# Optimization experiments

Measured on AMD Instinct MI355X. Metric: run time of the kernel, lower is better.

The kernel has to match this reference:

```python
import jax, jax.numpy as jnp
import numpy as np

EPS = 1e-6
BASE_LR = 0.01
MAX_GRAD_NORM = 1.0
CHUNK = 32


def _rms(x, w):
    return x * jax.lax.rsqrt(jnp.mean(x * x, axis=-1, keepdims=True) + EPS) * w


def _mem_fwd(p, x):
    # Memory MLP: linear -> silu -> linear -> RMSNorm -> residual. x: [D]
    h = jax.nn.silu(p['W1'] @ x)
    o = p['W2'] @ h
    return x + _rms(o, p['ln'])


def _loss(p, k, v, w):
    pred = _mem_fwd(p, k)
    return jnp.mean((v - pred) ** 2 * w)


def _binop(a, b):
    # Mamba-like: (a_j*a_i, kv_j + a_j*kv_i)  == torch.addcmul(kv_j, a_j, kv_i)
    (ai, ki), (aj, kj) = a, b
    return (aj * ai, kj + aj * ki)


def _scan_update(past_s, past_m, g, eta, alpha):
    # past_s/past_m: [B,*shape]; g: [B,C,*shape]; eta/alpha: [B,C]
    ext = (1,) * (g.ndim - 2)
    eta_b = eta.reshape(eta.shape + ext)
    alpha_b = alpha.reshape(alpha.shape + ext)
    ones = jnp.ones_like(eta_b[:, :1])
    a = jnp.concatenate([ones, eta_b], axis=1)
    kv = jnp.concatenate([past_s[:, None], -g], axis=1)
    _, s = jax.lax.associative_scan(_binop, (a, kv), axis=1)  # S_t = eta_t*S_{t-1} - g_t
    beta = jnp.concatenate([ones, 1.0 - alpha_b], axis=1)
    mem = jnp.concatenate([past_m[:, None], s[:, 1:]], axis=1)
    _, m = jax.lax.associative_scan(_binop, (beta, mem), axis=1)  # M_t = beta_t*M_{t-1} + S_t
    return s[:, -1], m[:, -1]


def _forward(x, wq, wk, wv, q_norm_w, k_norm_w, alpha_w, theta_w, eta_w, mem_w1, mem_w2, mem_ln):
    B, S, D = x.shape
    NC = S // CHUNK
    params = {'W1': jnp.broadcast_to(mem_w1, (B,) + mem_w1.shape),
              'W2': jnp.broadcast_to(mem_w2, (B,) + mem_w2.shape),
              'ln': jnp.broadcast_to(mem_ln, (B,) + mem_ln.shape)}
    surpr = jax.tree.map(jnp.zeros_like, params)
    xc_all = x.reshape(B, NC, CHUNK, D).transpose(1, 0, 2, 3)  # [NC,B,C,D]
    # per-sample, per-token grad of the TTT loss w.r.t. memory params
    grad_fn = jax.vmap(jax.vmap(jax.grad(_loss), in_axes=(None, 0, 0, 0)),
                       in_axes=(0, 0, 0, 0))

    def step(carry, xc):
        params, surpr = carry
        k = _rms(jax.nn.silu(xc @ wk.T), k_norm_w)      # [B,C,D]
        v = jax.nn.silu(xc @ wv.T)                       # [B,C,D]
        theta = BASE_LR * jax.nn.sigmoid(xc @ theta_w.T)  # [B,C,1] adaptive lr as loss weight
        alpha = jax.nn.sigmoid(xc @ alpha_w.T)[..., 0]     # [B,C] forget gate
        eta = jax.nn.sigmoid(xc @ eta_w.T)[..., 0]         # [B,C] momentum decay
        g = grad_fn(params, k, v, theta)                  # leaves [B,C,*shape]
        # global grad-norm clip per (b, t)
        sq = sum(jnp.sum(gi * gi, axis=tuple(range(2, gi.ndim)))
                 for gi in jax.tree.leaves(g))
        coef = jnp.minimum(MAX_GRAD_NORM / (jnp.sqrt(sq) + 1e-6), 1.0)
        g = jax.tree.map(lambda gi: gi * coef.reshape(coef.shape + (1,) * (gi.ndim - 2)), g)
        new_s, new_p = {}, {}
        for n in params:
            s_n, m_n = _scan_update(surpr[n], params[n], g[n], eta, alpha)
            new_s[n], new_p[n] = s_n, m_n
        return (new_p, new_s), None

    (params, surpr), _ = jax.lax.scan(step, (params, surpr), xc_all)
    # retrieve from the final memory weights
    q = _rms(jax.nn.silu(x @ wq.T), q_norm_w)
    h = jax.nn.silu(jnp.einsum('bsd,bid->bsi', q, params['W1']))
    o = jnp.einsum('bsi,bdi->bsd', h, params['W2'])
    out = q + _rms(o, params['ln'][:, None, :])
    return out


def setup_inputs() -> dict:
    key = jax.random.key(0)
    ks = jax.random.split(key, 12)
    B, S, D, I = 4, 512, 512, 1024

    def xavier(k, shape):
        fan = shape[-1] + shape[-2] if len(shape) > 1 else 2 * shape[-1]
        return jax.random.uniform(k, shape, jnp.float32, -1.0, 1.0) * jnp.sqrt(6.0 / fan)

    return {
        'x': jax.random.normal(ks[0], (B, S, D), jnp.float32),
        'wq': xavier(ks[1], (D, D)),
        'wk': xavier(ks[2], (D, D)),
        'wv': xavier(ks[3], (D, D)),
        'q_norm_w': jnp.ones((D,), jnp.float32),
        'k_norm_w': jnp.ones((D,), jnp.float32),
        'alpha_w': xavier(ks[4], (1, D)),
        'theta_w': xavier(ks[5], (1, D)),
        'eta_w': xavier(ks[6], (1, D)),
        'mem_w1': xavier(ks[7], (I, D)),
        'mem_w2': xavier(ks[8], (D, I)),
        'mem_ln': jnp.ones((D,), jnp.float32),
    }


def reference(x, wq, wk, wv, q_norm_w, k_norm_w, alpha_w, theta_w, eta_w, mem_w1, mem_w2, mem_ln):
    return _forward(x, wq, wk, wv, q_norm_w, k_norm_w, alpha_w, theta_w, eta_w,
                    mem_w1, mem_w2, mem_ln)
```

## Files before the change

kernel.cpp:

```cpp
#include <hip/hip_runtime.h>
#include <hip/hip_bf16.h>

#define B_ 4
#define S_ 512
#define D_ 512
#define I_ 1024
#define C_ 32
#define NC_ 16

#define KBUF (B_*S_*D_)
#define STSZ (B_*I_*D_)
#define HSZ  (B_*I_*C_)
#define DOSZ (B_*C_*D_)
#define OFF_K    0
#define OFF_V    (OFF_K + KBUF)
#define OFF_Q    (OFF_V + KBUF)
#define OFF_TH   (OFF_Q + KBUF)
#define OFF_AL   (OFF_TH + B_*S_)
#define OFF_ET   (OFF_AL + B_*S_)
#define OFF_KN2  (OFF_ET + B_*S_)
#define OFF_SLN  (OFF_KN2 + B_*S_)
#define OFF_MLN  (OFF_SLN + B_*D_)
#define OFF_H2   (OFF_MLN + B_*D_)
#define OFF_Z1   (OFF_H2 + 2*HSZ)
#define OFF_DHP  (OFF_Z1 + HSZ)
#define OFF_DO   (OFF_DHP + HSZ)
#define OFF_DLN  (OFF_DO + DOSZ)
#define OFF_OB   (OFF_DLN + DOSZ)
#define OFF_SLAB (OFF_OB + DOSZ)
#define SLABSTR  256
#define OFF_TICK (OFF_SLAB + NC_*B_*SLABSTR)
#define OFF_FLAG (OFF_TICK + 64)
#define OFF_ORET (OFF_FLAG + 16)
#define OFF_BST  (OFF_ORET + KBUF)
#define OFF_KBFf (OFF_BST + 2*STSZ)
#define OFF_KBTf (OFF_KBFf + KBUF/2)
#define OFF_HIT  (OFF_KBTf + KBUF/2)
#define OFF_HTI  (OFF_HIT + HSZ)
#define OFF_DOB  (OFF_HTI + HSZ)
#define OFF_DOT  (OFF_DOB + DOSZ/2)

typedef __attribute__((ext_vector_type(8))) short s8v;
typedef __attribute__((ext_vector_type(4))) float f4v;

__device__ __forceinline__ float bf2f(__hip_bfloat16 v){ return __bfloat162float(v); }
__device__ __forceinline__ float bfu2f(unsigned short u){ return __uint_as_float(((unsigned)u)<<16); }
__device__ __forceinline__ unsigned short f2bfu(float f){
  unsigned x = __float_as_uint(f);
  return (unsigned short)((x + 0x7FFFu + ((x>>16)&1u)) >> 16);
}
__device__ __forceinline__ float4 u42f4(ushort4 u){
  float4 r; r.x=bfu2f(u.x); r.y=bfu2f(u.y); r.z=bfu2f(u.z); r.w=bfu2f(u.w); return r;
}
__device__ __forceinline__ ushort4 f42u4(float4 v){
  ushort4 r; r.x=f2bfu(v.x); r.y=f2bfu(v.y); r.z=f2bfu(v.z); r.w=f2bfu(v.w); return r;
}
__device__ __forceinline__ float ldin(const void* p, size_t i, int f){
  return f ? ((const float*)p)[i] : bf2f(((const __hip_bfloat16*)p)[i]);
}
__device__ __forceinline__ float4 ld4g(const void* p, size_t i, int f){
  if(f) return ((const float4*)p)[i>>2];
  return u42f4(((const ushort4*)p)[i>>2]);
}
__device__ __forceinline__ void unp8(uint4 u, float* f){
  f[0]=bfu2f((unsigned short)(u.x&0xffffu)); f[1]=bfu2f((unsigned short)(u.x>>16));
  f[2]=bfu2f((unsigned short)(u.y&0xffffu)); f[3]=bfu2f((unsigned short)(u.y>>16));
  f[4]=bfu2f((unsigned short)(u.z&0xffffu)); f[5]=bfu2f((unsigned short)(u.z>>16));
  f[6]=bfu2f((unsigned short)(u.w&0xffffu)); f[7]=bfu2f((unsigned short)(u.w>>16));
}
__device__ __forceinline__ uint4 pck8(const float* f){
  uint4 u;
  u.x = (unsigned)f2bfu(f[0]) | ((unsigned)f2bfu(f[1])<<16);
  u.y = (unsigned)f2bfu(f[2]) | ((unsigned)f2bfu(f[3])<<16);
  u.z = (unsigned)f2bfu(f[4]) | ((unsigned)f2bfu(f[5])<<16);
  u.w = (unsigned)f2bfu(f[6]) | ((unsigned)f2bfu(f[7])<<16);
  return u;
}

__device__ __forceinline__ float blockReduceSum(float v, float* sm){
  #pragma unroll
  for(int o=32;o>0;o>>=1) v += __shfl_down(v,o,64);
  int wid = threadIdx.x>>6, lane = threadIdx.x&63;
  __syncthreads();
  if(lane==0) sm[wid]=v;
  __syncthreads();
  return sm[0]+sm[1]+sm[2]+sm[3];
}

__global__ void d0_detect(const void* __restrict__ x, float* __restrict__ ws){
  __shared__ int cnt;
  if(threadIdx.x==0) cnt=0;
  __syncthreads();
  unsigned w = ((const unsigned*)x)[(size_t)threadIdx.x*931 + 17];
  int e = (w>>7)&0xFF;
  if(e>=110 && e<=140) atomicAdd(&cnt,1);
  __syncthreads();
  if(threadIdx.x==0) ((int*)(ws+OFF_FLAG))[0] = (cnt<32) ? 1 : 0;
}

__global__ void p0_init(float* __restrict__ ws, const void* __restrict__ w1,
                        const void* __restrict__ w2, const void* __restrict__ ln){
  int f = ((const int*)(ws+OFF_FLAG))[0];
  unsigned short* bst = (unsigned short*)(ws + OFF_BST);
  size_t id = (size_t)blockIdx.x*blockDim.x + threadIdx.x;
  size_t stride = (size_t)gridDim.x*blockDim.x;
  ushort4 z4 = {0,0,0,0};
  for(size_t t4=id; t4<(size_t)(STSZ/4); t4+=stride){
    size_t e4 = t4 % (size_t)(I_*D_/4);
    *(ushort4*)(bst + (size_t)STSZ + t4*4)   = f42u4(ld4g(w1, e4*4, f));
    *(ushort4*)(bst + (size_t)3*STSZ + t4*4) = f42u4(ld4g(w2, e4*4, f));
    *(ushort4*)(bst + t4*4) = z4;
    *(ushort4*)(bst + (size_t)2*STSZ + t4*4) = z4;
  }
  for(size_t t=id; t<(size_t)(B_*D_); t+=stride){
    ws[OFF_MLN+t] = ldin(ln,t % D_,f);
    ws[OFF_SLN+t] = 0.f;
  }
  for(size_t t=id; t<(size_t)(NC_*B_*SLABSTR); t+=stride) ws[OFF_SLAB+t]=0.f;
  int* tick = (int*)(ws + OFF_TICK);
  for(size_t t=id; t<64; t+=stride) tick[t]=0;
}

__global__ void __launch_bounds__(256) cvt_in(const void* __restrict__ x,
                    const void* __restrict__ wk, const void* __restrict__ wv,
                    const void* __restrict__ wq, float* __restrict__ ws){
  int f = ((const int*)(ws+OFF_FLAG))[0];
  unsigned short* xbf = (unsigned short*)(ws + OFF_ORET);
  unsigned short* wbf = (unsigned short*)(ws + OFF_KBFf);
  size_t id = (size_t)blockIdx.x*blockDim.x + threadIdx.x;
  size_t stride = (size_t)gridDim.x*blockDim.x;
  for(size_t t4=id; t4<(size_t)(KBUF/4); t4+=stride)
    *(ushort4*)(xbf + t4*4) = f42u4(ld4g(x, t4*4, f));
  for(size_t t4=id; t4<(size_t)(3*D_*D_/4); t4+=stride){
    int pid = (int)(t4 / (D_*D_/4));
    size_t e4 = t4 % (size_t)(D_*D_/4);
    const void* W = (pid==0)?wk:((pid==1)?wv:wq);
    *(ushort4*)(wbf + t4*4) = f42u4(ld4g(W, e4*4, f));
  }
}

__global__ void __launch_bounds__(256) p1a(float* __restrict__ ws){
  const unsigned short* xbf = (const unsigned short*)(ws + OFF_ORET);
  const unsigned short* wbf = (const unsigned short*)(ws + OFF_KBFf);
  int pid = blockIdx.z;
  float* outp = ws + ((pid==0)?OFF_K:((pid==1)?OFF_V:OFF_Q));
  const unsigned short* W = wbf + (size_t)pid*D_*D_;
  int r0 = blockIdx.x*64, j0 = blockIdx.y*64;
  int w = threadIdx.x>>6, lane = threadIdx.x&63;
  int col = lane&15, lg = lane>>4;
  f4v acc[4] = {{0,0,0,0},{0,0,0,0},{0,0,0,0},{0,0,0,0}};
  for(int k0=0;k0<512;k0+=32){
    s8v bB = __builtin_bit_cast(s8v, *(const uint4*)(W + (size_t)(j0 + w*16 + col)*512 + k0 + lg*8));
    #pragma unroll
    for(int rg=0;rg<4;rg++){
      s8v aA = __builtin_bit_cast(s8v, *(const uint4*)(xbf + (size_t)(r0 + rg*16 + col)*512 + k0 + lg*8));
      acc[rg] = __builtin_amdgcn_mfma_f32_16x16x32_bf16(aA, bB, acc[rg], 0,0,0);
    }
  }
  #pragma unroll
  for(int rg=0;rg<4;rg++)
    #pragma unroll
    for(int j=0;j<4;j++){
      float z = acc[rg][j];
      outp[(size_t)(r0 + rg*16 + lg*4 + j)*512 + j0 + w*16 + col] = z/(1.f+expf(-z));
    }
}

__global__ void __launch_bounds__(256) p1b(const void* __restrict__ x,
                    const void* __restrict__ kn,
                    const void* __restrict__ qn,
                    const void* __restrict__ aw,
                    const void* __restrict__ tw,
                    const void* __restrict__ ew,
                    float* __restrict__ ws){
  int f = ((const int*)(ws+OFF_FLAG))[0];
  int tok = blockIdx.x; int tid = threadIdx.x;
  __shared__ float sm[8];
  float* krow = ws + OFF_K + (size_t)tok*512;
  float* qrow = ws + OFF_Q + (size_t)tok*512;
  float a = krow[tid], b = krow[tid+256];
  float ss = blockReduceSum(a*a+b*b, sm);
  float n = rsqrtf(ss*(1.f/512.f) + 1e-6f);
  float k1v = a*n*ldin(kn,tid,f);
  float k2v = b*n*ldin(kn,tid+256,f);
  krow[tid]=k1v; krow[tid+256]=k2v;
  float kn2 = blockReduceSum(k1v*k1v+k2v*k2v, sm);
  if(tid==0) ws[OFF_KN2+tok]=kn2;
  a = qrow[tid]; b = qrow[tid+256];
  ss = blockReduceSum(a*a+b*b, sm);
  n = rsqrtf(ss*(1.f/512.f)+1e-6f);
  qrow[tid]=a*n*ldin(qn,tid,f);
  qrow[tid+256]=b*n*ldin(qn,tid+256,f);
  float x1=ldin(x,(size_t)tok*512+tid,f), x2=ldin(x,(size_t)tok*512+tid+256,f);
  float td = blockReduceSum(x1*ldin(tw,tid,f) + x2*ldin(tw,tid+256,f), sm);
  float ad = blockReduceSum(x1*ldin(aw,tid,f) + x2*ldin(aw,tid+256,f), sm);
  float ed = blockReduceSum(x1*ldin(ew,tid,f) + x2*ldin(ew,tid+256,f), sm);
  if(tid==0){
    ws[OFF_TH+tok] = 0.01f/(1.f+expf(-td));
    ws[OFF_AL+tok] = 1.f/(1.f+expf(-ad));
    ws[OFF_ET+tok] = 1.f/(1.f+expf(-ed));
  }
}

__global__ void __launch_bounds__(256) tr_k(float* __restrict__ ws){
  unsigned short* kbf = (unsigned short*)(ws + OFF_KBFf);
  unsigned short* kbt = (unsigned short*)(ws + OFF_KBTf);
  int b = blockIdx.z, st = blockIdx.y, dt = blockIdx.x;
  int s0 = st*64, d0 = dt*64;
  __shared__ unsigned short t[64][72];
  int tid = threadIdx.x;
  #pragma unroll
  for(int q=0;q<4;q++){
    int idx = tid + q*256; int r = idx>>4, cq = idx&15;
    float4 v = *(const float4*)(ws + OFF_K + ((size_t)(b*512 + s0 + r))*512 + d0 + cq*4);
    ushort4 u; u.x=f2bfu(v.x); u.y=f2bfu(v.y); u.z=f2bfu(v.z); u.w=f2bfu(v.w);
    *(ushort4*)&t[r][cq*4] = u;
    *(ushort4*)(kbf + ((size_t)(b*512 + s0 + r))*512 + d0 + cq*4) = u;
  }
  __syncthreads();
  #pragma unroll
  for(int q=0;q<4;q++){
    int idx = tid + q*256; int d = idx>>4, sq = idx&15;
    ushort4 u; u.x=t[sq*4+0][d]; u.y=t[sq*4+1][d]; u.z=t[sq*4+2][d]; u.w=t[sq*4+3][d];
    *(ushort4*)(kbt + ((size_t)(b*512 + d0 + d))*512 + s0 + sq*4) = u;
  }
}

__global__ void __launch_bounds__(256) k1_w1(float* __restrict__ ws, int c){
  unsigned short* bsw1 = (unsigned short*)(ws + OFF_BST);
  unsigned short* bmw1 = bsw1 + STSZ;
  const unsigned short* kbf = (const unsigned short*)(ws + OFF_KBFf);
  const unsigned short* kbt = (const unsigned short*)(ws + OFF_KBTf);
  int b = blockIdx.y, bx = blockIdx.x, tid = threadIdx.x;
  __shared__ float sE[32], sC[32], scal[3];
  if(c>0){
    const float* slab = ws + OFF_SLAB + ((long)(c-1)*B_ + b)*SLABSTR;
    if(tid<32){ sE[tid]=slab[128+tid]; sC[tid]=slab[160+tid]; }
    if(tid>=32 && tid<35) scal[tid-32]=slab[192+(tid-32)];
  }
  __syncthreads();
  float PE = c>0? scal[0]:1.f, PB = c>0? scal[1]:1.f, Q = c>0? scal[2]:0.f;
  if(bx==64){
    if(c>0){
      for(int d=tid; d<512; d+=256){
        float gE=0,gC=0;
        for(int u=0;u<32;u++){
          float dl = ws[OFF_DLN + ((size_t)(b*32+u))*512 + d];
          gE += sE[u]*dl; gC += sC[u]*dl;
        }
        size_t ix = OFF_SLN + (size_t)b*512 + d;
        float sv=ws[ix], mv=ws[ix + (OFF_MLN-OFF_SLN)];
        ws[ix] = PE*sv - gE;
        ws[ix + (OFF_MLN-OFF_SLN)] = PB*mv + Q*sv - gC;
      }
    }
    return;
  }
  __shared__ __align__(16) float gbf[4][2][16][36];
  __shared__ __align__(16) unsigned short ztile[4][16][40];
  __shared__ __align__(16) float zred[4][16][32];
  __shared__ float hredL[32];
  int w = tid>>6, lane = tid&63;
  int i0 = bx*16;
  int col = lane&15, lg = lane>>4;
  int rr = lane>>2, c0 = (lane&3)*8;
  s8v aE = {}, aC = {};
  if(c>0){
    const float* dp = ws + OFF_DHP + ((size_t)(b*I_ + i0 + col))*32 + lg*8;
    float4 dv0 = *(const float4*)dp;
    float4 dv1 = *(const float4*)(dp+4);
    float dv[8] = {dv0.x,dv0.y,dv0.z,dv0.w,dv1.x,dv1.y,dv1.z,dv1.w};
    #pragma unroll
    for(int j=0;j<8;j++){
      aE[j] = (short)f2bfu(sE[lg*8+j]*dv[j]);
      aC[j] = (short)f2bfu(sC[lg*8+j]*dv[j]);
    }
  }
  f4v zacc0 = {0.f,0.f,0.f,0.f}, zacc1 = {0.f,0.f,0.f,0.f};
  const int d0w = w*128;
  const size_t srowbase = ((size_t)(b*I_ + i0))*512;
  const size_t kprow = (size_t)(c-1)*32;
  for(int sl=0; sl<4; sl++){
    int dbase = d0w + sl*32;
    size_t gaddr = srowbase + (size_t)rr*512 + dbase + c0;
    if(c>0){
      #pragma unroll
      for(int t2=0;t2<2;t2++){
        int dt = dbase + t2*16;
        const unsigned short* kp = kbt + ((size_t)(b*512 + dt + col))*512 + kprow + lg*8;
        s8v kB = __builtin_bit_cast(s8v, *(const uint4*)kp);
        f4v zero4 = {0.f,0.f,0.f,0.f};
        f4v gE4 = __builtin_amdgcn_mfma_f32_16x16x32_bf16(aE, kB, zero4, 0,0,0);
        f4v gC4 = __builtin_amdgcn_mfma_f32_16x16x32_bf16(aC, kB, zero4, 0,0,0);
        #pragma unroll
        for(int j=0;j<4;j++){
          gbf[w][0][lg*4+j][t2*16+col] = gE4[j];
          gbf[w][1][lg*4+j][t2*16+col] = gC4[j];
        }
      }
      uint4 su = *(uint4*)(bsw1 + gaddr);
      uint4 mu = *(uint4*)(bmw1 + gaddr);
      float s8[8], m8[8];
      unp8(su, s8); unp8(mu, m8);
      float ns[8], nmv[8];
      #pragma unroll
      for(int j=0;j<8;j++){
        float ge = gbf[w][0][rr][c0+j];
        float gc = gbf[w][1][rr][c0+j];
        ns[j]  = PE*s8[j] - ge;
        nmv[j] = PB*m8[j] + Q*s8[j] - gc;
      }
      *(uint4*)(bsw1 + gaddr) = pck8(ns);
      uint4 nmu = pck8(nmv);
      *(uint4*)(bmw1 + gaddr) = nmu;
      *(uint4*)&ztile[w][rr][c0] = nmu;
    } else {
      uint4 mu = *(uint4*)(bmw1 + gaddr);
      *(uint4*)&ztile[w][rr][c0] = mu;
    }
    if(c<16){
      s8v mA = __builtin_bit_cast(s8v, *(const uint4*)&ztile[w][col][lg*8]);
      const unsigned short* kc0 = kbf + ((size_t)(b*512 + c*32 + col))*512 + dbase + lg*8;
      s8v kB0 = __builtin_bit_cast(s8v, *(const uint4*)kc0);
      s8v kB1 = __builtin_bit_cast(s8v, *(const uint4*)(kc0 + (size_t)16*512));
      zacc0 = __builtin_amdgcn_mfma_f32_16x16x32_bf16(mA, kB0, zacc0, 0,0,0);
      zacc1 = __builtin_amdgcn_mfma_f32_16x16x32_bf16(mA, kB1, zacc1, 0,0,0);
    }
  }
  if(c<16){
    #pragma unroll
    for(int j=0;j<4;j++){
      zred[w][lg*4+j][col]    = zacc0[j];
      zred[w][lg*4+j][16+col] = zacc1[j];
    }
    if(tid<32) hredL[tid]=0.f;
    __syncthreads();
    unsigned short* hit = (unsigned short*)(ws + OFF_HIT) + (size_t)(c&1)*HSZ;
    unsigned short* hti = (unsigned short*)(ws + OFF_HTI) + (size_t)(c&1)*HSZ;
    #pragma unroll
    for(int e=0;e<2;e++){
      int idx = tid*2+e; int row = idx>>5, t = idx&31;
      float z = zred[0][row][t]+zred[1][row][t]+zred[2][row][t]+zred[3][row][t];
      size_t zb = ((size_t)(b*I_ + i0 + row))*32 + t;
      ws[OFF_Z1+zb] = z;
      float h = z/(1.f+expf(-z));
      unsigned short hb = f2bfu(h);
      hit[zb] = hb;
      hti[((size_t)(b*C_+t))*I_ + i0 + row] = hb;
      atomicAdd(&hredL[t], h*h);
    }
    __syncthreads();
    if(tid<32) atomicAdd(ws + OFF_SLAB + ((size_t)c*B_ + b)*SLABSTR + tid, hredL[tid]);
  }
}

__global__ void __launch_bounds__(256) k2_w2(float* __restrict__ ws, int c){
  unsigned short* bsw2 = (unsigned short*)(ws + OFF_BST) + (size_t)2*STSZ;
  unsigned short* bmw2 = bsw2 + STSZ;
  const unsigned short* hitp = (const unsigned short*)(ws + OFF_HIT) + (size_t)((c-1)&1)*HSZ;
  const unsigned short* htic = (const unsigned short*)(ws + OFF_HTI) + (size_t)(c&1)*HSZ;
  const unsigned short* dotb = (const unsigned short*)(ws + OFF_DOT);
  int b = blockIdx.y, bx = blockIdx.x, tid = threadIdx.x;
  int d0 = bx*16;
  __shared__ float sE[32], sC[32], scal[3];
  __shared__ __align__(16) float gbf[4][2][16][36];
  __shared__ __align__(16) unsigned short ztile[4][16][40];
  __shared__ __align__(16) float ored[4][16][32];
  if(c>0){
    const float* slab = ws + OFF_SLAB + ((long)(c-1)*B_+b)*SLABSTR;
    if(tid<32){ sE[tid]=slab[128+tid]; sC[tid]=slab[160+tid]; }
    if(tid>=32&&tid<35) scal[tid-32]=slab[192+tid-32];
  }
  __syncthreads();
  float PE = c>0?scal[0]:1.f, PB=c>0?scal[1]:1.f, Q=c>0?scal[2]:0.f;
  int w = tid>>6, lane = tid&63;
  int col = lane&15, lg = lane>>4;
  int rr = lane>>2, c0 = (lane&3)*8;
  s8v aE = {}, aC = {};
  if(c>0){
    const unsigned short* dp = dotb + ((size_t)(b*D_ + d0 + col))*32 + lg*8;
    float dv[8]; unp8(*(const uint4*)dp, dv);
    #pragma unroll
    for(int j=0;j<8;j++){
      aE[j] = (short)f2bfu(sE[lg*8+j]*dv[j]);
      aC[j] = (short)f2bfu(sC[lg*8+j]*dv[j]);
    }
  }
  f4v oacc0 = {0.f,0.f,0.f,0.f}, oacc1 = {0.f,0.f,0.f,0.f};
  const size_t srowbase = ((size_t)(b*D_ + d0))*1024;
  size_t ga0 = srowbase + (size_t)rr*1024 + w*256 + c0;
  uint4 su={0,0,0,0}, mu, svn=su, mvn;
  if(c>0) su = *(uint4*)(bsw2 + ga0);
  mu = *(uint4*)(bmw2 + ga0);
  for(int sl=0; sl<8; sl++){
    int ibase = w*256 + sl*32;
    size_t gaddr = srowbase + (size_t)rr*1024 + ibase + c0;
    if(sl<7){
      if(c>0) svn = *(uint4*)(bsw2 + gaddr + 32);
      mvn = *(uint4*)(bmw2 + gaddr + 32);
    }
    if(c>0){
      #pragma unroll
      for(int t2=0;t2<2;t2++){
        const unsigned short* hp = hitp + ((size_t)(b*I_ + ibase + t2*16 + col))*32 + lg*8;
        s8v hB = __builtin_bit_cast(s8v, *(const uint4*)hp);
        f4v zero4 = {0.f,0.f,0.f,0.f};
        f4v gE4 = __builtin_amdgcn_mfma_f32_16x16x32_bf16(aE, hB, zero4, 0,0,0);
        f4v gC4 = __builtin_amdgcn_mfma_f32_16x16x32_bf16(aC, hB, zero4, 0,0,0);
        #pragma unroll
        for(int j=0;j<4;j++){
          gbf[w][0][lg*4+j][t2*16+col] = gE4[j];
          gbf[w][1][lg*4+j][t2*16+col] = gC4[j];
        }
      }
      float s8[8], m8[8];
      unp8(su, s8); unp8(mu, m8);
      float ns[8], nmv[8];
      #pragma unroll
      for(int j=0;j<8;j++){
        ns[j]  = PE*s8[j] - gbf[w][0][rr][c0+j];
        nmv[j] = PB*m8[j] + Q*s8[j] - gbf[w][1][rr][c0+j];
      }
      *(uint4*)(bsw2 + gaddr) = pck8(ns);
      uint4 nmu = pck8(nmv);
      *(uint4*)(bmw2 + gaddr) = nmu;
      *(uint4*)&ztile[w][rr][c0] = nmu;
    } else {
      *(uint4*)&ztile[w][rr][c0] = mu;
    }
    if(c<16){
      s8v mA = __builtin_bit_cast(s8v, *(const uint4*)&ztile[w][col][lg*8]);
      const unsigned short* hb = htic + ((size_t)(b*C_+col))*I_ + ibase + lg*8;
      s8v hB0 = __builtin_bit_cast(s8v, *(const uint4*)hb);
      s8v hB1 = __builtin_bit_cast(s8v, *(const uint4*)(hb + (size_t)16*I_));
      oacc0 = __builtin_amdgcn_mfma_f32_16x16x32_bf16(mA, hB0, oacc0, 0,0,0);
      oacc1 = __builtin_amdgcn_mfma_f32_16x16x32_bf16(mA, hB1, oacc1, 0,0,0);
    }
    su = svn; mu = mvn;
  }
  if(c<16){
    #pragma unroll
    for(int j=0;j<4;j++){
      ored[w][lg*4+j][col]    = oacc0[j];
      ored[w][lg*4+j][16+col] = oacc1[j];
    }
    __syncthreads();
    #pragma unroll
    for(int e=0;e<2;e++){
      int idx = tid*2+e; int row = idx>>5, t = idx&31;
      float o = ored[0][row][t]+ored[1][row][t]+ored[2][row][t]+ored[3][row][t];
      ws[OFF_OB + ((size_t)(b*C_+t))*512 + d0 + row] = o;
    }
  }
}

__global__ void __launch_bounds__(256) k3_rms(float* __restrict__ ws, int c){
  int t = blockIdx.x, b = blockIdx.y, tid=threadIdx.x;
  __shared__ float sm[8];
  int tok = b*S_ + c*32 + t;
  const float* orow = ws + OFF_OB + ((size_t)(b*32+t))*512;
  const float* krow = ws + OFF_K + (size_t)tok*512;
  const float* vrow = ws + OFF_V + (size_t)tok*512;
  const float* lrow = ws + OFF_MLN + (size_t)b*512;
  float th = ws[OFF_TH + tok];
  float o1=orow[tid], o2=orow[tid+256];
  float mu = blockReduceSum(o1*o1+o2*o2, sm)*(1.f/512.f);
  float n = rsqrtf(mu + 1e-6f);
  float l1=lrow[tid], l2=lrow[tid+256];
  float k1=krow[tid], k2=krow[tid+256];
  float v1=vrow[tid], v2=vrow[tid+256];
  float c2 = 2.f*th*(1.f/512.f);
  float u1 = c2*(k1 + o1*n*l1 - v1);
  float u2 = c2*(k2 + o2*n*l2 - v2);
  float s1 = blockReduceSum(u1*l1*o1 + u2*l2*o2, sm);
  float dln1 = u1*o1*n, dln2v = u2*o2*n;
  float f = n*n*n*s1*(1.f/512.f);
  float do1 = n*l1*u1 - f*o1;
  float do2 = n*l2*u2 - f*o2;
  float don2 = blockReduceSum(do1*do1+do2*do2, sm);
  float dl2s = blockReduceSum(dln1*dln1+dln2v*dln2v, sm);
  float* dorow = ws + OFF_DO + ((size_t)(b*32+t))*512;
  float* dlrow = ws + OFF_DLN + ((size_t)(b*32+t))*512;
  dorow[tid]=do1; dorow[tid+256]=do2;
  dlrow[tid]=dln1; dlrow[tid+256]=dln2v;
  unsigned short* dob = (unsigned short*)(ws + OFF_DOB);
  unsigned short* dotb = (unsigned short*)(ws + OFF_DOT);
  dob[((size_t)(b*C_+t))*512 + tid]       = f2bfu(do1);
  dob[((size_t)(b*C_+t))*512 + tid + 256] = f2bfu(do2);
  dotb[((size_t)(b*D_ + tid))*32 + t]       = f2bfu(do1);
  dotb[((size_t)(b*D_ + tid + 256))*32 + t] = f2bfu(do2);
  if(tid==0){
    float* slab = ws + OFF_SLAB + ((size_t)c*B_+b)*SLABSTR;
    slab[64+t]=don2; slab[96+t]=dl2s;
  }
}

__global__ void __launch_bounds__(256) k4_dh(float* __restrict__ ws, int c){
  unsigned short* bmw2 = (unsigned short*)(ws + OFF_BST) + (size_t)3*STSZ;
  const unsigned short* dob = (const unsigned short*)(ws + OFF_DOB);
  int bx = blockIdx.x, b = blockIdx.y, tid = threadIdx.x;
  int i0 = bx*16;
  __shared__ unsigned short m2u[16][520];
  __shared__ __align__(16) float dred[4][16][32];
  __shared__ float red[32], coefl[32], bsufl[32];
  __shared__ int lastf;
  #pragma unroll
  for(int q=0;q<4;q++){
    int idx = tid + q*256; int d = idx>>1, half = idx&1;
    uint4 v = *(const uint4*)(bmw2 + ((size_t)(b*D_+d))*1024 + i0 + half*8);
    unsigned short tmp[8]; *(uint4*)tmp = v;
    #pragma unroll
    for(int jj=0;jj<8;jj++) m2u[half*8+jj][d] = tmp[jj];
  }
  if(tid<32) red[tid]=0.f;
  __syncthreads();
  int w = tid>>6, lane = tid&63;
  int col = lane&15, lg = lane>>4;
  f4v acc0 = {0.f,0.f,0.f,0.f}, acc1 = {0.f,0.f,0.f,0.f};
  #pragma unroll
  for(int ks=0;ks<4;ks++){
    int k0 = w*128 + ks*32;
    s8v mA = __builtin_bit_cast(s8v, *(const uint4*)&m2u[col][k0 + lg*8]);
    const unsigned short* dp = dob + ((size_t)(b*C_+col))*512 + k0 + lg*8;
    s8v dB0 = __builtin_bit_cast(s8v, *(const uint4*)dp);
    s8v dB1 = __builtin_bit_cast(s8v, *(const uint4*)(dp + (size_t)16*512));
    acc0 = __builtin_amdgcn_mfma_f32_16x16x32_bf16(mA, dB0, acc0, 0,0,0);
    acc1 = __builtin_amdgcn_mfma_f32_16x16x32_bf16(mA, dB1, acc1, 0,0,0);
  }
  #pragma unroll
  for(int j=0;j<4;j++){
    dred[w][lg*4+j][col]    = acc0[j];
    dred[w][lg*4+j][16+col] = acc1[j];
  }
  __syncthreads();
  #pragma unroll
  for(int e=0;e<2;e++){
    int idx = tid*2+e; int row = idx>>5, t = idx&31;
    float dh = dred[0][row][t]+dred[1][row][t]+dred[2][row][t]+dred[3][row][t];
    size_t zb = ((size_t)(b*I_ + i0 + row))*32 + t;
    float z = ws[OFF_Z1+zb];
    float s = 1.f/(1.f+expf(-z));
    float dp_ = dh * s*(1.f + z*(1.f-s));
    ws[OFF_DHP+zb] = dp_;
    atomicAdd(&red[t], dp_*dp_);
  }
  __syncthreads();
  float* slab = ws + OFF_SLAB + ((size_t)c*B_+b)*SLABSTR;
  if(tid<32) atomicAdd(&slab[32+tid], red[tid]);
  __threadfence();
  __syncthreads();
  if(tid==0){
    int* tick = (int*)(ws+OFF_TICK);
    lastf = (atomicAdd(&tick[c*B_+b],1) == 63) ? 1 : 0;
  }
  __syncthreads();
  if(!lastf) return;
  if(tid<32){
    float sqd = atomicAdd(&slab[32+tid], 0.f);
    float hn  = atomicAdd(&slab[0+tid], 0.f);
    float don2 = slab[64+tid], dl2 = slab[96+tid];
    float kn2 = ws[OFF_KN2 + b*S_ + c*32 + tid];
    float sq = sqd*kn2 + don2*hn + dl2;
    coefl[tid] = fminf(1.f/(sqrtf(sq)+1e-6f), 1.f);
  }
  __syncthreads();
  if(tid==0){
    const float* eta = ws + OFF_ET + b*S_ + c*32;
    const float* alp = ws + OFF_AL + b*S_ + c*32;
    float Esuf=1.f, Bsuf=1.f, cu=1.f;
    for(int u=31;u>=0;u--){
      if(u<31){
        float e1 = eta[u+1], b1 = 1.f-alp[u+1];
        Esuf *= e1; Bsuf *= b1;
        cu = Bsuf + e1*cu;
      }
      bsufl[u]=Bsuf;
      slab[128+u] = Esuf*coefl[u];
      slab[160+u] = cu*coefl[u];
    }
    float PE = Esuf*eta[0];
    float PB = Bsuf*(1.f-alp[0]);
    float Q=0.f, Epre=1.f;
    for(int t2=0;t2<32;t2++){ Epre *= eta[t2]; Q += bsufl[t2]*Epre; }
    slab[192]=PE; slab[193]=PB; slab[194]=Q;
  }
}

__global__ void __launch_bounds__(256) cvt_q(float* __restrict__ ws){
  unsigned short* qbf = (unsigned short*)(ws + OFF_V);
  size_t id = (size_t)blockIdx.x*blockDim.x + threadIdx.x;
  float4 v = *(const float4*)(ws + OFF_Q + id*4);
  *(ushort4*)(qbf + id*4) = f42u4(v);
}

__global__ void __launch_bounds__(256) r1_gemm(float* __restrict__ ws){
  const unsigned short* qbf = (const unsigned short*)(ws + OFF_V);
  const unsigned short* bmw1 = (const unsigned short*)(ws + OFF_BST) + STSZ;
  unsigned short* hqb = (unsigned short*)(ws + OFF_K);
  int b = blockIdx.z;
  int s0 = blockIdx.x*64, i0 = blockIdx.y*64;
  int w = threadIdx.x>>6, lane = threadIdx.x&63;
  int col = lane&15, lg = lane>>4;
  const unsigned short* qb = qbf + (size_t)b*S_*D_;
  const unsigned short* w1b = bmw1 + (size_t)b*I_*D_;
  f4v acc[4] = {{0,0,0,0},{0,0,0,0},{0,0,0,0},{0,0,0,0}};
  for(int k0=0;k0<512;k0+=32){
    s8v bB = __builtin_bit_cast(s8v, *(const uint4*)(w1b + (size_t)(i0 + w*16 + col)*512 + k0 + lg*8));
    #pragma unroll
    for(int rg=0;rg<4;rg++){
      s8v aA = __builtin_bit_cast(s8v, *(const uint4*)(qb + (size_t)(s0 + rg*16 + col)*512 + k0 + lg*8));
      acc[rg] = __builtin_amdgcn_mfma_f32_16x16x32_bf16(aA, bB, acc[rg], 0,0,0);
    }
  }
  unsigned short* hb = hqb + (size_t)b*S_*I_;
  #pragma unroll
  for(int rg=0;rg<4;rg++)
    #pragma unroll
    for(int j=0;j<4;j++){
      float z = acc[rg][j];
      hb[(size_t)(s0 + rg*16 + lg*4 + j)*1024 + i0 + w*16 + col] = f2bfu(z/(1.f+expf(-z)));
    }
}

__global__ void __launch_bounds__(256) r2_gemm(float* __restrict__ ws){
  const unsigned short* hqb = (const unsigned short*)(ws + OFF_K);
  const unsigned short* bmw2 = (const unsigned short*)(ws + OFF_BST) + (size_t)3*STSZ;
  int b=blockIdx.z;
  int s0=blockIdx.x*64, d0=blockIdx.y*64;
  int w = threadIdx.x>>6, lane = threadIdx.x&63;
  int col = lane&15, lg = lane>>4;
  const unsigned short* hb = hqb + (size_t)b*S_*I_;
  const unsigned short* w2b = bmw2 + (size_t)b*D_*I_;
  f4v acc[4] = {{0,0,0,0},{0,0,0,0},{0,0,0,0},{0,0,0,0}};
  for(int k0=0;k0<1024;k0+=32){
    s8v bB = __builtin_bit_cast(s8v, *(const uint4*)(w2b + (size_t)(d0 + w*16 + col)*1024 + k0 + lg*8));
    #pragma unroll
    for(int rg=0;rg<4;rg++){
      s8v aA = __builtin_bit_cast(s8v, *(const uint4*)(hb + (size_t)(s0 + rg*16 + col)*1024 + k0 + lg*8));
      acc[rg] = __builtin_amdgcn_mfma_f32_16x16x32_bf16(aA, bB, acc[rg], 0,0,0);
    }
  }
  float* od = ws + OFF_ORET + (size_t)b*S_*D_;
  #pragma unroll
  for(int rg=0;rg<4;rg++)
    #pragma unroll
    for(int j=0;j<4;j++)
      od[(size_t)(s0 + rg*16 + lg*4 + j)*512 + d0 + w*16 + col] = acc[rg][j];
}

__global__ void __launch_bounds__(256) r3_out(float* __restrict__ ws, void* __restrict__ out){
  int f = ((const int*)(ws+OFF_FLAG))[0];
  int tok=blockIdx.x, tid=threadIdx.x;
  int b = tok >> 9;
  __shared__ float sm[8];
  const float* orow = ws + OFF_ORET + (size_t)tok*512;
  const float* qrow = ws + OFF_Q + (size_t)tok*512;
  const float* lrow = ws + OFF_MLN + (size_t)b*512;
  float o1=orow[tid], o2=orow[tid+256];
  float mu = blockReduceSum(o1*o1+o2*o2, sm)*(1.f/512.f);
  float n = rsqrtf(mu+1e-6f);
  float r1v = qrow[tid]     + o1*n*lrow[tid];
  float r2v = qrow[tid+256] + o2*n*lrow[tid+256];
  if(f){
    ((float*)out)[(size_t)tok*512+tid]     = r1v;
    ((float*)out)[(size_t)tok*512+tid+256] = r2v;
  } else {
    ((__hip_bfloat16*)out)[(size_t)tok*512+tid]     = __float2bfloat16(r1v);
    ((__hip_bfloat16*)out)[(size_t)tok*512+tid+256] = __float2bfloat16(r2v);
  }
}

extern "C" void kernel_launch(void* const* d_in, const int* in_sizes, int n_in,
                              void* d_out, int out_size, void* d_ws, size_t ws_size,
                              hipStream_t stream) {
  const void* x  = d_in[0];
  const void* wq = d_in[1];
  const void* wk = d_in[2];
  const void* wv = d_in[3];
  const void* qn = d_in[4];
  const void* kn = d_in[5];
  const void* aw = d_in[6];
  const void* tw = d_in[7];
  const void* ew = d_in[8];
  const void* w1 = d_in[9];
  const void* w2 = d_in[10];
  const void* ln = d_in[11];
  float* ws = (float*)d_ws;

  d0_detect<<<1,64,0,stream>>>(x, ws);
  p0_init<<<2048,256,0,stream>>>(ws, w1, w2, ln);
  cvt_in<<<2048,256,0,stream>>>(x, wk, wv, wq, ws);
  p1a<<<dim3(32,8,3),256,0,stream>>>(ws);
  p1b<<<2048,256,0,stream>>>(x, kn, qn, aw, tw, ew, ws);
  tr_k<<<dim3(8,8,4),256,0,stream>>>(ws);
  for(int c=0;c<=16;c++){
    k1_w1<<<dim3(65,4),256,0,stream>>>(ws, c);
    k2_w2<<<dim3(32,4),256,0,stream>>>(ws, c);
    if(c<16){
      k3_rms<<<dim3(32,4),256,0,stream>>>(ws, c);
      k4_dh<<<dim3(64,4),256,0,stream>>>(ws, c);
    }
  }
  cvt_q<<<1024,256,0,stream>>>(ws);
  r1_gemm<<<dim3(8,16,4),256,0,stream>>>(ws);
  r2_gemm<<<dim3(8,8,4),256,0,stream>>>(ws);
  r3_out<<<2048,256,0,stream>>>(ws, d_out);
}
```

Baseline: 1.056 ms.

## Fuse RMS-backward into dh kernel and merge conversion launches

```diff
diff --git a/kernel.cpp b/kernel.cpp
--- a/kernel.cpp
+++ b/kernel.cpp
@@ -30,7 +30,8 @@
 #define OFF_SLAB (OFF_OB + DOSZ)
 #define SLABSTR  256
 #define OFF_TICK (OFF_SLAB + NC_*B_*SLABSTR)
-#define OFF_FLAG (OFF_TICK + 64)
+#define OFF_TK2  (OFF_TICK + 64)
+#define OFF_FLAG (OFF_TK2 + 128)
 #define OFF_ORET (OFF_FLAG + 16)
 #define OFF_BST  (OFF_ORET + KBUF)
 #define OFF_KBFf (OFF_BST + 2*STSZ)
@@ -87,6 +88,12 @@
   return sm[0]+sm[1]+sm[2]+sm[3];
 }
 
+__device__ __forceinline__ float wred(float v){
+  #pragma unroll
+  for(int o=32;o>0;o>>=1) v += __shfl_xor(v,o,64);
+  return v;
+}
+
 __global__ void d0_detect(const void* __restrict__ x, float* __restrict__ ws){
   __shared__ int cnt;
   if(threadIdx.x==0) cnt=0;
@@ -99,7 +106,9 @@
 }
 
 __global__ void p0_init(float* __restrict__ ws, const void* __restrict__ w1,
-                        const void* __restrict__ w2, const void* __restrict__ ln){
+                        const void* __restrict__ w2, const void* __restrict__ ln,
+                        const void* __restrict__ x, const void* __restrict__ wk,
+                        const void* __restrict__ wv, const void* __restrict__ wq){
   int f = ((const int*)(ws+OFF_FLAG))[0];
   unsigned short* bst = (unsigned short*)(ws + OFF_BST);
   size_t id = (size_t)blockIdx.x*blockDim.x + threadIdx.x;
@@ -112,23 +121,8 @@
     *(ushort4*)(bst + t4*4) = z4;
     *(ushort4*)(bst + (size_t)2*STSZ + t4*4) = z4;
   }
-  for(size_t t=id; t<(size_t)(B_*D_); t+=stride){
-    ws[OFF_MLN+t] = ldin(ln,t % D_,f);
-    ws[OFF_SLN+t] = 0.f;
-  }
-  for(size_t t=id; t<(size_t)(NC_*B_*SLABSTR); t+=stride) ws[OFF_SLAB+t]=0.f;
-  int* tick = (int*)(ws + OFF_TICK);
-  for(size_t t=id; t<64; t+=stride) tick[t]=0;
-}
-
-__global__ void __launch_bounds__(256) cvt_in(const void* __restrict__ x,
-                    const void* __restrict__ wk, const void* __restrict__ wv,
-                    const void* __restrict__ wq, float* __restrict__ ws){
-  int f = ((const int*)(ws+OFF_FLAG))[0];
   unsigned short* xbf = (unsigned short*)(ws + OFF_ORET);
   unsigned short* wbf = (unsigned short*)(ws + OFF_KBFf);
-  size_t id = (size_t)blockIdx.x*blockDim.x + threadIdx.x;
-  size_t stride = (size_t)gridDim.x*blockDim.x;
   for(size_t t4=id; t4<(size_t)(KBUF/4); t4+=stride)
     *(ushort4*)(xbf + t4*4) = f42u4(ld4g(x, t4*4, f));
   for(size_t t4=id; t4<(size_t)(3*D_*D_/4); t4+=stride){
@@ -137,6 +131,13 @@
     const void* W = (pid==0)?wk:((pid==1)?wv:wq);
     *(ushort4*)(wbf + t4*4) = f42u4(ld4g(W, e4*4, f));
   }
+  for(size_t t=id; t<(size_t)(B_*D_); t+=stride){
+    ws[OFF_MLN+t] = ldin(ln,t % D_,f);
+    ws[OFF_SLN+t] = 0.f;
+  }
+  for(size_t t=id; t<(size_t)(NC_*B_*SLABSTR); t+=stride) ws[OFF_SLAB+t]=0.f;
+  int* tick = (int*)(ws + OFF_TICK);
+  for(size_t t=id; t<192; t+=stride) tick[t]=0;
 }
 
 __global__ void __launch_bounds__(256) p1a(float* __restrict__ ws){
@@ -189,8 +190,12 @@
   a = qrow[tid]; b = qrow[tid+256];
   ss = blockReduceSum(a*a+b*b, sm);
   n = rsqrtf(ss*(1.f/512.f)+1e-6f);
-  qrow[tid]=a*n*ldin(qn,tid,f);
-  qrow[tid+256]=b*n*ldin(qn,tid+256,f);
+  float q1 = a*n*ldin(qn,tid,f);
+  float q2 = b*n*ldin(qn,tid+256,f);
+  qrow[tid]=q1; qrow[tid+256]=q2;
+  unsigned short* qbf = (unsigned short*)(ws + OFF_ORET + KBUF/2);
+  qbf[(size_t)tok*512+tid]     = f2bfu(q1);
+  qbf[(size_t)tok*512+tid+256] = f2bfu(q2);
   float x1=ldin(x,(size_t)tok*512+tid,f), x2=ldin(x,(size_t)tok*512+tid+256,f);
   float td = blockReduceSum(x1*ldin(tw,tid,f) + x2*ldin(tw,tid+256,f), sm);
   float ad = blockReduceSum(x1*ldin(aw,tid,f) + x2*ldin(aw,tid+256,f), sm);
@@ -454,56 +459,16 @@
   }
 }
 
-__global__ void __launch_bounds__(256) k3_rms(float* __restrict__ ws, int c){
-  int t = blockIdx.x, b = blockIdx.y, tid=threadIdx.x;
-  __shared__ float sm[8];
-  int tok = b*S_ + c*32 + t;
-  const float* orow = ws + OFF_OB + ((size_t)(b*32+t))*512;
-  const float* krow = ws + OFF_K + (size_t)tok*512;
-  const float* vrow = ws + OFF_V + (size_t)tok*512;
-  const float* lrow = ws + OFF_MLN + (size_t)b*512;
-  float th = ws[OFF_TH + tok];
-  float o1=orow[tid], o2=orow[tid+256];
-  float mu = blockReduceSum(o1*o1+o2*o2, sm)*(1.f/512.f);
-  float n = rsqrtf(mu + 1e-6f);
-  float l1=lrow[tid], l2=lrow[tid+256];
-  float k1=krow[tid], k2=krow[tid+256];
-  float v1=vrow[tid], v2=vrow[tid+256];
-  float c2 = 2.f*th*(1.f/512.f);
-  float u1 = c2*(k1 + o1*n*l1 - v1);
-  float u2 = c2*(k2 + o2*n*l2 - v2);
-  float s1 = blockReduceSum(u1*l1*o1 + u2*l2*o2, sm);
-  float dln1 = u1*o1*n, dln2v = u2*o2*n;
-  float f = n*n*n*s1*(1.f/512.f);
-  float do1 = n*l1*u1 - f*o1;
-  float do2 = n*l2*u2 - f*o2;
-  float don2 = blockReduceSum(do1*do1+do2*do2, sm);
-  float dl2s = blockReduceSum(dln1*dln1+dln2v*dln2v, sm);
-  float* dorow = ws + OFF_DO + ((size_t)(b*32+t))*512;
-  float* dlrow = ws + OFF_DLN + ((size_t)(b*32+t))*512;
-  dorow[tid]=do1; dorow[tid+256]=do2;
-  dlrow[tid]=dln1; dlrow[tid+256]=dln2v;
-  unsigned short* dob = (unsigned short*)(ws + OFF_DOB);
-  unsigned short* dotb = (unsigned short*)(ws + OFF_DOT);
-  dob[((size_t)(b*C_+t))*512 + tid]       = f2bfu(do1);
-  dob[((size_t)(b*C_+t))*512 + tid + 256] = f2bfu(do2);
-  dotb[((size_t)(b*D_ + tid))*32 + t]       = f2bfu(do1);
-  dotb[((size_t)(b*D_ + tid + 256))*32 + t] = f2bfu(do2);
-  if(tid==0){
-    float* slab = ws + OFF_SLAB + ((size_t)c*B_+b)*SLABSTR;
-    slab[64+t]=don2; slab[96+t]=dl2s;
-  }
-}
-
-__global__ void __launch_bounds__(256) k4_dh(float* __restrict__ ws, int c){
+__global__ void __launch_bounds__(256) k34(float* __restrict__ ws, int c){
   unsigned short* bmw2 = (unsigned short*)(ws + OFF_BST) + (size_t)3*STSZ;
-  const unsigned short* dob = (const unsigned short*)(ws + OFF_DOB);
   int bx = blockIdx.x, b = blockIdx.y, tid = threadIdx.x;
   int i0 = bx*16;
-  __shared__ unsigned short m2u[16][520];
+  __shared__ __align__(16) unsigned short m2u[16][520];
+  __shared__ __align__(16) unsigned short doL[32][520];
   __shared__ __align__(16) float dred[4][16][32];
   __shared__ float red[32], coefl[32], bsufl[32];
   __shared__ int lastf;
+  float* slab = ws + OFF_SLAB + ((size_t)c*B_+b)*SLABSTR;
   #pragma unroll
   for(int q=0;q<4;q++){
     int idx = tid + q*256; int d = idx>>1, half = idx&1;
@@ -513,17 +478,67 @@
     for(int jj=0;jj<8;jj++) m2u[half*8+jj][d] = tmp[jj];
   }
   if(tid<32) red[tid]=0.f;
-  __syncthreads();
   int w = tid>>6, lane = tid&63;
+  {
+    const float* lrow = ws + OFF_MLN + (size_t)b*512;
+    float l8[8];
+    *(float4*)&l8[0] = *(const float4*)(lrow + lane*8);
+    *(float4*)&l8[4] = *(const float4*)(lrow + lane*8 + 4);
+    for(int tt=0; tt<8; tt++){
+      int t = w*8 + tt;
+      int tok = b*S_ + c*32 + t;
+      const float* orow = ws + OFF_OB + ((size_t)(b*32+t))*512;
+      const float* krow = ws + OFF_K + (size_t)tok*512;
+      const float* vrow = ws + OFF_V + (size_t)tok*512;
+      float th = ws[OFF_TH + tok];
+      float o8[8], k8[8], v8[8];
+      *(float4*)&o8[0] = *(const float4*)(orow+lane*8); *(float4*)&o8[4] = *(const float4*)(orow+lane*8+4);
+      *(float4*)&k8[0] = *(const float4*)(krow+lane*8); *(float4*)&k8[4] = *(const float4*)(krow+lane*8+4);
+      *(float4*)&v8[0] = *(const float4*)(vrow+lane*8); *(float4*)&v8[4] = *(const float4*)(vrow+lane*8+4);
+      float ss = 0.f;
+      #pragma unroll
+      for(int j=0;j<8;j++) ss += o8[j]*o8[j];
+      float mu = wred(ss)*(1.f/512.f);
+      float n = rsqrtf(mu + 1e-6f);
+      float c2 = 2.f*th*(1.f/512.f);
+      float u8[8]; float s1p = 0.f;
+      #pragma unroll
+      for(int j=0;j<8;j++){
+        u8[j] = c2*(k8[j] + o8[j]*n*l8[j] - v8[j]);
+        s1p += u8[j]*l8[j]*o8[j];
+      }
+      float s1 = wred(s1p);
+      float fr = n*n*n*s1*(1.f/512.f);
+      float do8[8], dln8[8]; float dd2=0.f, dl2=0.f;
+      #pragma unroll
+      for(int j=0;j<8;j++){
+        do8[j]  = n*l8[j]*u8[j] - fr*o8[j];
+        dln8[j] = u8[j]*o8[j]*n;
+        dd2 += do8[j]*do8[j]; dl2 += dln8[j]*dln8[j];
+      }
+      float don2 = wred(dd2), dl2s = wred(dl2);
+      *(uint4*)&doL[t][lane*8] = pck8(do8);
+      if(bx==0){
+        float* dlrow = ws + OFF_DLN + ((size_t)(b*32+t))*512;
+        *(float4*)(dlrow+lane*8)   = *(float4*)&dln8[0];
+        *(float4*)(dlrow+lane*8+4) = *(float4*)&dln8[4];
+        unsigned short* dotw = (unsigned short*)(ws + OFF_DOT);
+        #pragma unroll
+        for(int j=0;j<8;j++)
+          dotw[((size_t)(b*D_ + lane*8 + j))*32 + t] = f2bfu(do8[j]);
+        if(lane==0){ atomicAdd(&slab[64+t], don2); atomicAdd(&slab[96+t], dl2s); }
+      }
+    }
+  }
+  __syncthreads();
   int col = lane&15, lg = lane>>4;
   f4v acc0 = {0.f,0.f,0.f,0.f}, acc1 = {0.f,0.f,0.f,0.f};
   #pragma unroll
   for(int ks=0;ks<4;ks++){
     int k0 = w*128 + ks*32;
-    s8v mA = __builtin_bit_cast(s8v, *(const uint4*)&m2u[col][k0 + lg*8]);
-    const unsigned short* dp = dob + ((size_t)(b*C_+col))*512 + k0 + lg*8;
-    s8v dB0 = __builtin_bit_cast(s8v, *(const uint4*)dp);
-    s8v dB1 = __builtin_bit_cast(s8v, *(const uint4*)(dp + (size_t)16*512));
+    s8v mA  = __builtin_bit_cast(s8v, *(const uint4*)&m2u[col][k0 + lg*8]);
+    s8v dB0 = __builtin_bit_cast(s8v, *(const uint4*)&doL[col][k0 + lg*8]);
+    s8v dB1 = __builtin_bit_cast(s8v, *(const uint4*)&doL[col+16][k0 + lg*8]);
     acc0 = __builtin_amdgcn_mfma_f32_16x16x32_bf16(mA, dB0, acc0, 0,0,0);
     acc1 = __builtin_amdgcn_mfma_f32_16x16x32_bf16(mA, dB1, acc1, 0,0,0);
   }
@@ -545,7 +560,6 @@
     atomicAdd(&red[t], dp_*dp_);
   }
   __syncthreads();
-  float* slab = ws + OFF_SLAB + ((size_t)c*B_+b)*SLABSTR;
   if(tid<32) atomicAdd(&slab[32+tid], red[tid]);
   __threadfence();
   __syncthreads();
@@ -558,7 +572,8 @@
   if(tid<32){
     float sqd = atomicAdd(&slab[32+tid], 0.f);
     float hn  = atomicAdd(&slab[0+tid], 0.f);
-    float don2 = slab[64+tid], dl2 = slab[96+tid];
+    float don2 = atomicAdd(&slab[64+tid], 0.f);
+    float dl2  = atomicAdd(&slab[96+tid], 0.f);
     float kn2 = ws[OFF_KN2 + b*S_ + c*32 + tid];
     float sq = sqd*kn2 + don2*hn + dl2;
     coefl[tid] = fminf(1.f/(sqrtf(sq)+1e-6f), 1.f);
@@ -586,15 +601,8 @@
   }
 }
 
-__global__ void __launch_bounds__(256) cvt_q(float* __restrict__ ws){
-  unsigned short* qbf = (unsigned short*)(ws + OFF_V);
-  size_t id = (size_t)blockIdx.x*blockDim.x + threadIdx.x;
-  float4 v = *(const float4*)(ws + OFF_Q + id*4);
-  *(ushort4*)(qbf + id*4) = f42u4(v);
-}
-
 __global__ void __launch_bounds__(256) r1_gemm(float* __restrict__ ws){
-  const unsigned short* qbf = (const unsigned short*)(ws + OFF_V);
+  const unsigned short* qbf = (const unsigned short*)(ws + OFF_ORET + KBUF/2);
   const unsigned short* bmw1 = (const unsigned short*)(ws + OFF_BST) + STSZ;
   unsigned short* hqb = (unsigned short*)(ws + OFF_K);
   int b = blockIdx.z;
@@ -688,20 +696,15 @@
   float* ws = (float*)d_ws;
 
   d0_detect<<<1,64,0,stream>>>(x, ws);
-  p0_init<<<2048,256,0,stream>>>(ws, w1, w2, ln);
-  cvt_in<<<2048,256,0,stream>>>(x, wk, wv, wq, ws);
+  p0_init<<<2048,256,0,stream>>>(ws, w1, w2, ln, x, wk, wv, wq);
   p1a<<<dim3(32,8,3),256,0,stream>>>(ws);
   p1b<<<2048,256,0,stream>>>(x, kn, qn, aw, tw, ew, ws);
   tr_k<<<dim3(8,8,4),256,0,stream>>>(ws);
   for(int c=0;c<=16;c++){
     k1_w1<<<dim3(65,4),256,0,stream>>>(ws, c);
     k2_w2<<<dim3(32,4),256,0,stream>>>(ws, c);
-    if(c<16){
-      k3_rms<<<dim3(32,4),256,0,stream>>>(ws, c);
-      k4_dh<<<dim3(64,4),256,0,stream>>>(ws, c);
-    }
-  }
-  cvt_q<<<1024,256,0,stream>>>(ws);
+    if(c<16) k34<<<dim3(64,4),256,0,stream>>>(ws, c);
+  }
   r1_gemm<<<dim3(8,16,4),256,0,stream>>>(ws);
   r2_gemm<<<dim3(8,8,4),256,0,stream>>>(ws);
   r3_out<<<2048,256,0,stream>>>(ws, d_out);
```

Result: slower. 1.404 ms (+32.9%).
